# Performance work log

Measured on AMD Instinct MI355X. Metric: run time of the kernel, lower is better.

Reference implementation:

```python
import jax, jax.numpy as jnp
import numpy as np

B, S, D = 16, 2048, 512
SEQ_START = 4
MAX_LEN = 1007
NUM_SEQ = MAX_LEN - SEQ_START  # 1003 rows in sequence_embeddings
VOCAB = 100


def setup_inputs() -> dict:
    key = jax.random.key(0)
    k_x, k_ids, k_pos, k_c, k_s = jax.random.split(key, 5)
    x = jax.random.normal(k_x, (B, S, D), dtype=jnp.float32)
    input_ids = jax.random.randint(k_ids, (B, S), 0, VOCAB, dtype=jnp.int64)
    start_token_id = 5
    # plant exactly one guaranteed start token per row at pos >= SEQ_START
    start_pos = jax.random.randint(k_pos, (B,), SEQ_START, S // 2, dtype=jnp.int64)
    input_ids = input_ids.at[jnp.arange(B), start_pos].set(start_token_id)
    control_emb = jax.random.normal(k_c, (SEQ_START, D), dtype=jnp.float32) * 0.02
    sequence_emb = jax.random.normal(k_s, (NUM_SEQ, D), dtype=jnp.float32) * 0.02
    return {"x": x, "input_ids": input_ids, "start_token_id": start_token_id,
            "control_emb": control_emb, "sequence_emb": sequence_emb}


def reference(x, input_ids, start_token_id, control_emb, sequence_emb):
    Bx, Sx, Dx = x.shape
    pos = jnp.arange(Sx)
    # control embeddings fill positions [0, SEQ_START)
    n_ctrl = control_emb.shape[0]
    ctrl_mask = pos < n_ctrl                                 # [S]
    ctrl_part = control_emb[jnp.clip(pos, 0, n_ctrl - 1)]    # [S, D]
    ctrl_part = jnp.where(ctrl_mask[:, None], ctrl_part, 0.0)
    # sequence embeddings: for each position i, rel = i - (last start pos <= i
    # with start pos >= SEQ_START); later starts overwrite earlier ones,
    # matching the torch loop's overwrite semantics.
    is_start = (input_ids == start_token_id) & (pos[None, :] >= SEQ_START)  # [B, S]
    marker = jnp.where(is_start, pos[None, :], -1)
    last_start = jax.lax.cummax(marker, axis=1)              # [B, S]
    rel = pos[None, :] - last_start                          # [B, S]
    n_seq = sequence_emb.shape[0]
    valid = (last_start >= 0) & (rel < n_seq)                # [B, S]
    seq_part = sequence_emb[jnp.clip(rel, 0, n_seq - 1)]     # [B, S, D]
    pos_emb = jnp.where(valid[:, :, None], seq_part, ctrl_part[None, :, :])
    return x + pos_emb
```

## Files before the change

kernel.cpp:

```cpp
#include <hip/hip_runtime.h>
#include <hip/hip_bf16.h>


#define S_LEN 2048
#define D_DIM 512
#define D4 (D_DIM / 4)
#define SEQ_START 4
#define NUM_SEQ 1003
#define SCAN_THREADS 256
#define CHUNK (S_LEN / SCAN_THREADS)

__global__ void __launch_bounds__(SCAN_THREADS)
alpe_scan_kernel(const int* __restrict__ ids,
                 const int* __restrict__ start_tok,
                 int* __restrict__ codes) {
    const int b = blockIdx.x;
    const int t = threadIdx.x;
    const int st = *start_tok;

    __shared__ int tmax[SCAN_THREADS];

    const int base = t * CHUNK;
    int local[CHUNK];
    int m = -1;
    #pragma unroll
    for (int k = 0; k < CHUNK; ++k) {
        const int j = base + k;
        const int id = ids[b * S_LEN + j];
        const int mk = (id == st && j >= SEQ_START) ? j : -1;
        local[k] = mk;
        m = max(m, mk);
    }
    tmax[t] = m;
    __syncthreads();

    for (int off = 1; off < SCAN_THREADS; off <<= 1) {
        const int other = (t >= off) ? tmax[t - off] : -1;
        __syncthreads();
        tmax[t] = max(tmax[t], other);
        __syncthreads();
    }
    int carry = (t == 0) ? -1 : tmax[t - 1];

    #pragma unroll
    for (int k = 0; k < CHUNK; ++k) {
        const int i = base + k;
        carry = max(carry, local[k]);
        int code;
        if (carry >= 0) {
            const int rel = i - carry;
            if (rel < NUM_SEQ) code = rel;
            else               code = (i < SEQ_START) ? (-2 - i) : -1;
        } else {
            code = (i < SEQ_START) ? (-2 - i) : -1;
        }
        codes[b * S_LEN + i] = code;
    }
}

__global__ void __launch_bounds__(256)
alpe_add_kernel(const float4* __restrict__ x,
                const float4* __restrict__ ctrl,
                const float4* __restrict__ seq,
                const int* __restrict__ codes,
                float4* __restrict__ out,
                int total) {
    int idx = blockIdx.x * blockDim.x + threadIdx.x;
    const int stride = gridDim.x * blockDim.x;
    for (; idx < total; idx += stride) {
        const int d4 = idx & (D4 - 1);
        const int bs = idx >> 7;
        const int code = codes[bs];
        const float4 xv = x[idx];
        float4 e = make_float4(0.f, 0.f, 0.f, 0.f);
        if (code >= 0) {
            e = seq[code * D4 + d4];
        } else if (code <= -2) {
            e = ctrl[(-2 - code) * D4 + d4];
        }
        out[idx] = make_float4(xv.x + e.x, xv.y + e.y, xv.z + e.z, xv.w + e.w);
    }
}

extern "C" void kernel_launch(void* const* d_in, const int* in_sizes, int n_in,
                              void* d_out, int out_size, void* d_ws, size_t ws_size,
                              hipStream_t stream) {
    const float* x          = (const float*)d_in[0];
    const int*   input_ids  = (const int*)d_in[1];
    const int*   start_tok  = (const int*)d_in[2];
    const float* ctrl       = (const float*)d_in[3];
    const float* seq        = (const float*)d_in[4];
    float*       out        = (float*)d_out;

    const int B = in_sizes[1] / S_LEN;
    int* codes = (int*)d_ws;

    alpe_scan_kernel<<<B, SCAN_THREADS, 0, stream>>>(input_ids, start_tok, codes);

    const int total = B * S_LEN * D4;
    const int blocks = 2048;
    alpe_add_kernel<<<blocks, 256, 0, stream>>>(
        (const float4*)x, (const float4*)ctrl, (const float4*)seq,
        codes, (float4*)out, total);
}
```

Measured before the change: 31.48 us.

## Fuse prefix-max scan into embedding add kernel with per-chunk redundant scan

```diff
diff --git a/kernel.cpp b/kernel.cpp
--- a/kernel.cpp
+++ b/kernel.cpp
@@ -7,99 +7,102 @@
 #define D4 (D_DIM / 4)
 #define SEQ_START 4
 #define NUM_SEQ 1003
-#define SCAN_THREADS 256
-#define CHUNK (S_LEN / SCAN_THREADS)
+#define CS 64
+#define NCHUNK (S_LEN / CS)
+#define THREADS 512
+#define NWAVE (THREADS / 64)
+#define PER (S_LEN / THREADS)
 
-__global__ void __launch_bounds__(SCAN_THREADS)
-alpe_scan_kernel(const int* __restrict__ ids,
-                 const int* __restrict__ start_tok,
-                 int* __restrict__ codes) {
-    const int b = blockIdx.x;
+typedef float f4 __attribute__((ext_vector_type(4)));
+
+__global__ void __launch_bounds__(THREADS)
+alpe_fused_kernel(const f4* __restrict__ x,
+                  const f4* __restrict__ ctrl,
+                  const f4* __restrict__ seq,
+                  const int* __restrict__ ids,
+                  const int* __restrict__ start_tok,
+                  f4* __restrict__ out) {
+    const int b   = blockIdx.x / NCHUNK;
+    const int cid = blockIdx.x % NCHUNK;
+    const int chunk_start = cid * CS;
     const int t = threadIdx.x;
     const int st = *start_tok;
 
-    __shared__ int tmax[SCAN_THREADS];
+    __shared__ int wmax[NWAVE];
+    __shared__ int codes_s[CS];
 
-    const int base = t * CHUNK;
-    int local[CHUNK];
     int m = -1;
     #pragma unroll
-    for (int k = 0; k < CHUNK; ++k) {
-        const int j = base + k;
-        const int id = ids[b * S_LEN + j];
-        const int mk = (id == st && j >= SEQ_START) ? j : -1;
-        local[k] = mk;
-        m = max(m, mk);
+    for (int k = 0; k < PER; ++k) {
+        const int j = t * PER + k;
+        if (j < chunk_start) {
+            const int id = ids[b * S_LEN + j];
+            if (id == st && j >= SEQ_START) m = max(m, j);
+        }
     }
-    tmax[t] = m;
+    #pragma unroll
+    for (int off = 32; off >= 1; off >>= 1)
+        m = max(m, __shfl_xor(m, off));
+    if ((t & 63) == 0) wmax[t >> 6] = m;
     __syncthreads();
 
-    for (int off = 1; off < SCAN_THREADS; off <<= 1) {
-        const int other = (t >= off) ? tmax[t - off] : -1;
-        __syncthreads();
-        tmax[t] = max(tmax[t], other);
-        __syncthreads();
+    if (t < 64) {
+        const int p = chunk_start + t;
+        const int id = ids[b * S_LEN + p];
+        int mk = (id == st && p >= SEQ_START) ? p : -1;
+        #pragma unroll
+        for (int off = 1; off < 64; off <<= 1) {
+            const int o = __shfl_up(mk, off);
+            if (t >= off) mk = max(mk, o);
+        }
+        int carry = -1;
+        #pragma unroll
+        for (int w = 0; w < NWAVE; ++w) carry = max(carry, wmax[w]);
+        const int last = max(mk, carry);
+        int code;
+        if (last >= 0) {
+            const int rel = p - last;
+            code = (rel < NUM_SEQ) ? rel : -1;
+        } else {
+            code = (p < SEQ_START) ? (-2 - p) : -1;
+        }
+        codes_s[t] = code;
     }
-    int carry = (t == 0) ? -1 : tmax[t - 1];
+    __syncthreads();
 
+    const size_t base4 = ((size_t)(b * S_LEN + chunk_start)) * D4;
     #pragma unroll
-    for (int k = 0; k < CHUNK; ++k) {
-        const int i = base + k;
-        carry = max(carry, local[k]);
-        int code;
-        if (carry >= 0) {
-            const int rel = i - carry;
-            if (rel < NUM_SEQ) code = rel;
-            else               code = (i < SEQ_START) ? (-2 - i) : -1;
-        } else {
-            code = (i < SEQ_START) ? (-2 - i) : -1;
-        }
-        codes[b * S_LEN + i] = code;
-    }
-}
-
-__global__ void __launch_bounds__(256)
-alpe_add_kernel(const float4* __restrict__ x,
-                const float4* __restrict__ ctrl,
-                const float4* __restrict__ seq,
-                const int* __restrict__ codes,
-                float4* __restrict__ out,
-                int total) {
-    int idx = blockIdx.x * blockDim.x + threadIdx.x;
-    const int stride = gridDim.x * blockDim.x;
-    for (; idx < total; idx += stride) {
-        const int d4 = idx & (D4 - 1);
-        const int bs = idx >> 7;
-        const int code = codes[bs];
-        const float4 xv = x[idx];
-        float4 e = make_float4(0.f, 0.f, 0.f, 0.f);
+    for (int it = 0; it < (CS * D4) / THREADS; ++it) {
+        const int j  = it * THREADS + t;
+        const int sl = j >> 7;
+        const int d4 = j & (D4 - 1);
+        const int code = codes_s[sl];
+        const f4 xv = __builtin_nontemporal_load(&x[base4 + j]);
+        f4 e = (f4){0.f, 0.f, 0.f, 0.f};
         if (code >= 0) {
             e = seq[code * D4 + d4];
         } else if (code <= -2) {
             e = ctrl[(-2 - code) * D4 + d4];
         }
-        out[idx] = make_float4(xv.x + e.x, xv.y + e.y, xv.z + e.z, xv.w + e.w);
+        const f4 r = xv + e;
+        __builtin_nontemporal_store(r, &out[base4 + j]);
     }
 }
 
 extern "C" void kernel_launch(void* const* d_in, const int* in_sizes, int n_in,
                               void* d_out, int out_size, void* d_ws, size_t ws_size,
                               hipStream_t stream) {
-    const float* x          = (const float*)d_in[0];
-    const int*   input_ids  = (const int*)d_in[1];
-    const int*   start_tok  = (const int*)d_in[2];
-    const float* ctrl       = (const float*)d_in[3];
-    const float* seq        = (const float*)d_in[4];
-    float*       out        = (float*)d_out;
+    const float* x         = (const float*)d_in[0];
+    const int*   input_ids = (const int*)d_in[1];
+    const int*   start_tok = (const int*)d_in[2];
+    const float* ctrl      = (const float*)d_in[3];
+    const float* seq       = (const float*)d_in[4];
+    float*       out       = (float*)d_out;
 
     const int B = in_sizes[1] / S_LEN;
-    int* codes = (int*)d_ws;
+    const int grid = B * NCHUNK;
 
-    alpe_scan_kernel<<<B, SCAN_THREADS, 0, stream>>>(input_ids, start_tok, codes);
-
-    const int total = B * S_LEN * D4;
-    const int blocks = 2048;
-    alpe_add_kernel<<<blocks, 256, 0, stream>>>(
-        (const float4*)x, (const float4*)ctrl, (const float4*)seq,
-        codes, (float4*)out, total);
+    alpe_fused_kernel<<<grid, THREADS, 0, stream>>>(
+        (const f4*)x, (const f4*)ctrl, (const f4*)seq,
+        input_ids, start_tok, (f4*)out);
 }
```

Result: no change. 31.89 us (+1.3%).
